# Optimization experiments

Hardware: AMD Instinct MI355X
Metric: run time of the kernel (lower is better)

## Reference

```python
import jax, jax.numpy as jnp
import numpy as np


def _conv(x, w, b=None, stride=1, pad=1):
    y = jax.lax.conv_general_dilated(x, w, (stride, stride), [(pad, pad), (pad, pad)],
                                     dimension_numbers=('NCHW', 'OIHW', 'NCHW'))
    return y if b is None else y + b[None, :, None, None]


def _relu(x):
    return jnp.maximum(x, 0.0)


def _slice(grid, guide):
    # grid: [N,C=12,D=8,Hg=16,Wg=16]; guide: [N,H,W] in [0,1]
    # Emulates F.grid_sample(5D, align_corners=False, padding_mode='border') with
    # coords (x=ww over Wg, y=hh over Hg, z=guide over D).
    N, C, D, Hg, Wg = grid.shape
    H, W = guide.shape[1], guide.shape[2]

    def unnorm(c, size):
        return jnp.clip(((c + 1.0) * size - 1.0) * 0.5, 0.0, size - 1.0)

    ix = unnorm(jnp.linspace(-1.0, 1.0, W), Wg)   # [W]
    iy = unnorm(jnp.linspace(-1.0, 1.0, H), Hg)   # [H]
    iz = unnorm(guide * 2.0 - 1.0, D)             # [N,H,W]
    x0f = jnp.floor(ix); y0f = jnp.floor(iy); z0f = jnp.floor(iz)
    wx = (ix - x0f)[None, :]   # [1,W]
    wy = (iy - y0f)[:, None]   # [H,1]
    wz = iz - z0f              # [N,H,W]
    x0 = jnp.clip(x0f.astype(jnp.int32), 0, Wg - 1); x1 = jnp.clip(x0 + 1, 0, Wg - 1)
    y0 = jnp.clip(y0f.astype(jnp.int32), 0, Hg - 1); y1 = jnp.clip(y0 + 1, 0, Hg - 1)
    z0 = jnp.clip(z0f.astype(jnp.int32), 0, D - 1);  z1 = jnp.clip(z0 + 1, 0, D - 1)

    def sample_one(g, z0n, z1n, wzn):
        # g: [C,D,Hg,Wg]; z0n,z1n,wzn: [H,W]
        def gat(zi, yi, xi):
            return g[:, zi, yi[:, None], xi[None, :]]  # [C,H,W]
        out = jnp.zeros((C, H, W), g.dtype)
        for zi, wzz in ((z0n, 1.0 - wzn), (z1n, wzn)):
            for yi, wyy in ((y0, 1.0 - wy), (y1, wy)):
                for xi, wxx in ((x0, 1.0 - wx), (x1, wx)):
                    out = out + (wzz * wyy * wxx)[None] * gat(zi, yi, xi)
        return out

    return jax.vmap(sample_one, in_axes=(0, 0, 0, 0))(grid, z0, z1, wz)  # [N,12,H,W]


def _forward(lowres, fullres, sw1, sb1, sw2, sb2, sw3, sb3, sw4, sb4,
             gw1, gb1, gw2, gb2, fw3, fb3, fw4, fb4, fw5, fb5,
             lw1, lb1, lw2, pw, pb, M, Mb, thr, slopes, gbias):
    N = lowres.shape[0]
    # Coefficients (low-res CNN)
    x = _relu(_conv(lowres, sw1, sb1, 2))
    x = _relu(_conv(x, sw2, sb2, 2))
    x = _relu(_conv(x, sw3, sb3, 2))
    x = _relu(_conv(x, sw4, sb4, 2))
    splat = x                                  # [N,64,16,16]
    x = _relu(_conv(x, gw1, gb1, 2))
    x = _relu(_conv(x, gw2, gb2, 2))           # [N,64,4,4]
    x = x.reshape(N, -1)
    x = _relu(x @ fw3.T + fb3)
    x = _relu(x @ fw4.T + fb4)
    glob = x @ fw5.T + fb5                     # [N,64]
    loc = _conv(_relu(_conv(splat, lw1, lb1)), lw2, None)
    fusion = _relu(loc + glob[:, :, None, None])
    grid = _conv(fusion, pw, pb, 1, 0).reshape(N, 12, 8, 16, 16)

    # Guide (full-res pointwise network)
    f = fullres.transpose(0, 2, 3, 1)          # [N,H,W,3]
    g = f @ M + Mb                             # [N,H,W,3]
    g = jnp.sum(slopes * _relu(g[..., None] - thr), axis=4)  # [N,H,W,3]
    guide = jnp.clip(jnp.mean(g, axis=3) + gbias, 0.0, 1.0)  # [N,H,W]

    sliced = _slice(grid, guide)               # [N,12,H,W]
    rr = jnp.sum(fullres * sliced[:, 0:3], axis=1) + sliced[:, 3]
    gg = jnp.sum(fullres * sliced[:, 4:7], axis=1) + sliced[:, 7]
    bb = jnp.sum(fullres * sliced[:, 8:11], axis=1) + sliced[:, 11]
    return jnp.stack([rr, gg, bb], axis=1)


def setup_inputs():
    key = jax.random.key(0)
    ks = jax.random.split(key, 32)
    r = lambda i, shape, s=0.1: jax.random.normal(ks[i], shape, jnp.float32) * s
    return {
        'lowres': jax.random.uniform(ks[0], (2, 3, 256, 256), dtype=jnp.float32),
        'fullres': jax.random.uniform(ks[1], (2, 3, 1024, 1024), dtype=jnp.float32),
        'sw1': r(2, (8, 3, 3, 3)),   'sb1': r(3, (8,), 0.01),
        'sw2': r(4, (16, 8, 3, 3)),  'sb2': r(5, (16,), 0.01),
        'sw3': r(6, (32, 16, 3, 3)), 'sb3': r(7, (32,), 0.01),
        'sw4': r(8, (64, 32, 3, 3)), 'sb4': r(9, (64,), 0.01),
        'gw1': r(10, (64, 64, 3, 3)), 'gb1': r(11, (64,), 0.01),
        'gw2': r(12, (64, 64, 3, 3)), 'gb2': r(13, (64,), 0.01),
        'fw3': r(14, (256, 1024), 0.05), 'fb3': r(15, (256,), 0.01),
        'fw4': r(16, (128, 256), 0.05),  'fb4': r(17, (128,), 0.01),
        'fw5': r(18, (64, 128), 0.05),   'fb5': r(19, (64,), 0.01),
        'lw1': r(20, (64, 64, 3, 3)), 'lb1': r(21, (64,), 0.01),
        'lw2': r(22, (64, 64, 3, 3)),
        'pw': r(23, (96, 64, 1, 1)), 'pb': r(24, (96,), 0.01),
        'M': jnp.eye(3, dtype=jnp.float32) + r(25, (3, 3), 0.0001),
        'Mb': jnp.zeros((3,), jnp.float32),
        'thr': jax.random.uniform(ks[26], (1, 1, 3, 16), dtype=jnp.float32),
        'slopes': r(27, (1, 1, 1, 3, 16), 0.3),
        'gbias': jnp.asarray(0.05, jnp.float32),
    }


def reference(lowres, fullres, sw1, sb1, sw2, sb2, sw3, sb3, sw4, sb4,
              gw1, gb1, gw2, gb2, fw3, fb3, fw4, fb4, fw5, fb5,
              lw1, lb1, lw2, pw, pb, M, Mb, thr, slopes, gbias):
    return _forward(lowres, fullres, sw1, sb1, sw2, sb2, sw3, sb3, sw4, sb4,
                    gw1, gb1, gw2, gb2, fw3, fb3, fw4, fb4, fw5, fb5,
                    lw1, lb1, lw2, pw, pb, M, Mb, thr, slopes, gbias)
```

## Files before the change

kernel.cpp:

```cpp
#include <hip/hip_runtime.h>


#define LUT_NB   512
#define LUT_LO   (-0.25f)
#define LUT_BIN  (1.5f / LUT_NB)
#define LUT_INV  (LUT_NB / 1.5f)

__global__ void __launch_bounds__(256) conv12_k(
    const float* __restrict__ lowres,
    const float* __restrict__ sw1, const float* __restrict__ sb1,
    const float* __restrict__ sw2, const float* __restrict__ sb2,
    const float* __restrict__ thr, const float* __restrict__ slp,
    const float* __restrict__ fw3, const float* __restrict__ fw4,
    const float* __restrict__ fw5,
    float* __restrict__ x2, float2* __restrict__ lut,
    float* __restrict__ fwt3, float* __restrict__ fwt4,
    float* __restrict__ fwt5)
{
    __shared__ float s_x1[9 * 9 * 8];
    const int tid  = threadIdx.x;
    const int n    = blockIdx.x >> 8;
    const int tile = blockIdx.x & 255;
    const int ty   = tile >> 4, tx = tile & 15;

    {
        int tg = blockIdx.x * 256 + tid;
        #pragma unroll
        for (int r = 0; r < 2; ++r) {
            int e = tg + r * 131072;
            int o = e & 255, k = e >> 8;
            fwt3[e] = fw3[o * 1024 + k];
        }
        if (tg < 32768) {
            int o = tg & 127, k = tg >> 7;
            fwt4[tg] = fw4[o * 256 + k];
        }
        if (tg < 8192) {
            int o = tg & 63, k = tg >> 6;
            fwt5[tg] = fw5[o * 128 + k];
        }
    }

    if (blockIdx.x == 0) {
        for (int e = tid; e < 3 * LUT_NB; e += 256) {
            int j = e >> 9;
            int i = e & (LUT_NB - 1);
            float xl = LUT_LO + i * LUT_BIN;
            float xh = xl + LUT_BIN;
            float a = 0.0f, c = 0.0f;
            #pragma unroll
            for (int k = 0; k < 16; ++k) {
                float tt = thr[j * 16 + k], ss = slp[j * 16 + k];
                a = fmaf(ss, fmaxf(xl - tt, 0.0f), a);
                c = fmaf(ss, fmaxf(xh - tt, 0.0f), c);
            }
            lut[e] = make_float2(a, c - a);
        }
    }

    const int b1h = 8 * ty - 1, b1w = 8 * tx - 1;

    for (int i = tid; i < 648; i += 256) {
        int c   = i & 7;
        int pos = i >> 3;
        int lw  = pos % 9, lh = pos / 9;
        int gh  = b1h + lh, gw = b1w + lw;
        float v = 0.0f;
        if (gh >= 0 && gh < 128 && gw >= 0 && gw < 128) {
            float acc = sb1[c];
            #pragma unroll
            for (int ci = 0; ci < 3; ++ci) {
                const float* ib = lowres + ((size_t)(n * 3 + ci)) * 65536;
                const float* wb = sw1 + ((size_t)c * 3 + ci) * 9;
                #pragma unroll
                for (int kh = 0; kh < 3; ++kh) {
                    int ih = 2 * gh - 1 + kh;
                    if (ih < 0 || ih >= 256) continue;
                    #pragma unroll
                    for (int kw = 0; kw < 3; ++kw) {
                        int iw = 2 * gw - 1 + kw;
                        if (iw < 0 || iw >= 256) continue;
                        acc = fmaf(ib[ih * 256 + iw], wb[kh * 3 + kw], acc);
                    }
                }
            }
            v = fmaxf(acc, 0.0f);
        }
        s_x1[i] = v;
    }
    __syncthreads();

    {
        int co  = tid & 15;
        int pos = tid >> 4;
        int ooh = pos >> 2, oow = pos & 3;
        int oh  = 4 * ty + ooh, ow = 4 * tx + oow;
        float acc = sb2[co];
        const float* wb = sw2 + (size_t)co * 72;
        #pragma unroll
        for (int kh = 0; kh < 3; ++kh) {
            #pragma unroll
            for (int kw = 0; kw < 3; ++kw) {
                const float* xp = &s_x1[((2 * ooh + kh) * 9 + (2 * oow + kw)) * 8];
                const float* wp = wb + kh * 3 + kw;
                #pragma unroll
                for (int ci = 0; ci < 8; ++ci)
                    acc = fmaf(xp[ci], wp[ci * 9], acc);
            }
        }
        x2[((size_t)(n * 64 + oh) * 64 + ow) * 16 + co] = fmaxf(acc, 0.0f);
    }
}

template <int CIN>
__global__ void convw_hwc_k(const float* __restrict__ in, const float* __restrict__ w,
                            const float* __restrict__ b, float* __restrict__ out,
                            int N, int Hin, int Win, int Cout, int Hout, int Wout,
                            int stride, int do_relu)
{
    constexpr int OPW = 64 / CIN;
    int lane = threadIdx.x & 63;
    int wid  = (blockIdx.x * blockDim.x + threadIdx.x) >> 6;
    int sub  = lane / CIN;
    int cl   = lane % CIN;
    int o    = wid * OPW + sub;
    int total = N * Hout * Wout * Cout;

    float acc = 0.0f;
    if (o < total) {
        int co  = o % Cout;
        int pix = o / Cout;
        int ow  = pix % Wout;
        int oh  = (pix / Wout) % Hout;
        int n   = pix / (Wout * Hout);
        const float* wb = w + ((size_t)co * CIN + cl) * 9;
        #pragma unroll
        for (int kh = 0; kh < 3; ++kh) {
            int ih = oh * stride - 1 + kh;
            if (ih < 0 || ih >= Hin) continue;
            const float* ib = in + (((size_t)(n * Hin + ih)) * Win) * CIN + cl;
            #pragma unroll
            for (int kw = 0; kw < 3; ++kw) {
                int iw = ow * stride - 1 + kw;
                if (iw < 0 || iw >= Win) continue;
                acc = fmaf(ib[(size_t)iw * CIN], wb[kh * 3 + kw], acc);
            }
        }
    }
    #pragma unroll
    for (int off = CIN / 2; off >= 1; off >>= 1)
        acc += __shfl_xor(acc, off, 64);

    if (o < total && cl == 0) {
        if (b) acc += b[o % Cout];
        if (do_relu) acc = fmaxf(acc, 0.0f);
        out[o] = acc;
    }
}

__device__ __forceinline__ void convw64_one(const float* __restrict__ in,
                                            const float* __restrict__ wgt,
                                            const float* __restrict__ bias,
                                            float* __restrict__ out,
                                            int o, int Hin, int Win, int Wout,
                                            int stride, bool relu, int lane)
{
    int co  = o & 63;
    int pix = o >> 6;
    int ow  = pix % Wout;
    int oh  = pix / Wout;
    const float* wb = wgt + ((size_t)co * 64 + lane) * 9;
    float acc = 0.0f;
    #pragma unroll
    for (int kh = 0; kh < 3; ++kh) {
        int ih = oh * stride - 1 + kh;
        if (ih < 0 || ih >= Hin) continue;
        const float* ib = in + ((size_t)ih * Win) * 64 + lane;
        #pragma unroll
        for (int kw = 0; kw < 3; ++kw) {
            int iw = ow * stride - 1 + kw;
            if (iw < 0 || iw >= Win) continue;
            acc = fmaf(ib[(size_t)iw * 64], wb[kh * 3 + kw], acc);
        }
    }
    #pragma unroll
    for (int off = 32; off >= 1; off >>= 1)
        acc += __shfl_xor(acc, off, 64);
    if (lane == 0) {
        if (bias) acc += bias[co];
        if (relu) acc = fmaxf(acc, 0.0f);
        out[o] = acc;
    }
}

__global__ void l1_g1_k(const float* __restrict__ splat,
                        const float* __restrict__ lw1, const float* __restrict__ lb1,
                        const float* __restrict__ gw1, const float* __restrict__ gb1,
                        float* __restrict__ l1, float* __restrict__ g1)
{
    int lane = threadIdx.x & 63;
    int W = (blockIdx.x * blockDim.x + threadIdx.x) >> 6;
    if (W < 32768) {
        int n = W >> 14, o = W & 16383;
        convw64_one(splat + (size_t)n * 16384, lw1, lb1, l1 + (size_t)n * 16384,
                    o, 16, 16, 16, 1, true, lane);
    } else {
        int W2 = W - 32768;
        if (W2 >= 8192) return;
        int n = W2 >> 12, o = W2 & 4095;
        convw64_one(splat + (size_t)n * 16384, gw1, gb1, g1 + (size_t)n * 4096,
                    o, 16, 16, 8, 2, true, lane);
    }
}

__global__ void loc_g2_k(const float* __restrict__ l1, const float* __restrict__ lw2,
                         const float* __restrict__ g1, const float* __restrict__ gw2,
                         const float* __restrict__ gb2,
                         float* __restrict__ loc, float* __restrict__ g2)
{
    int lane = threadIdx.x & 63;
    int W = (blockIdx.x * blockDim.x + threadIdx.x) >> 6;
    if (W < 32768) {
        int n = W >> 14, o = W & 16383;
        convw64_one(l1 + (size_t)n * 16384, lw2, nullptr, loc + (size_t)n * 16384,
                    o, 16, 16, 16, 1, false, lane);
    } else {
        int W2 = W - 32768;
        if (W2 >= 2048) return;
        int n = W2 >> 10, o = W2 & 1023;
        convw64_one(g1 + (size_t)n * 4096, gw2, gb2, g2 + (size_t)n * 1024,
                    o, 8, 8, 4, 2, true, lane);
    }
}

__global__ void __launch_bounds__(1024) fcfusion96_k(
    const float* __restrict__ g2,
    const float* __restrict__ fwt3, const float* __restrict__ fb3,
    const float* __restrict__ fwt4, const float* __restrict__ fb4,
    const float* __restrict__ fwt5, const float* __restrict__ fb5,
    const float* __restrict__ loc,
    const float* __restrict__ pw, const float* __restrict__ pb,
    float* __restrict__ gridc)
{
    __shared__ float s_in[1024];
    __shared__ float s_p[1024];
    __shared__ float s_f3[256];
    __shared__ float s_f4[128];
    __shared__ float s_gl[64];

    const int tid = threadIdx.x;
    const int n   = blockIdx.x / 48;
    const int q   = blockIdx.x % 48;

    if (tid < 1024)
        s_in[tid] = g2[(size_t)n * 1024 + (tid & 15) * 64 + (tid >> 4)];
    __syncthreads();

    {
        int o = tid & 255, part = tid >> 8;
        const float* wp = fwt3 + (size_t)(part * 256) * 256 + o;
        const float* ip = s_in + part * 256;
        float acc = 0.0f;
        #pragma unroll 8
        for (int k = 0; k < 256; ++k)
            acc = fmaf(wp[k * 256], ip[k], acc);
        s_p[tid] = acc;
    }
    __syncthreads();
    if (tid < 256)
        s_f3[tid] = fmaxf(fb3[tid] + s_p[tid] + s_p[256 + tid] +
                          s_p[512 + tid] + s_p[768 + tid], 0.0f);
    __syncthreads();

    if (tid < 512) {
        int o = tid & 127, part = tid >> 7;
        const float* wp = fwt4 + (size_t)(part * 64) * 128 + o;
        const float* ip = s_f3 + part * 64;
        float acc = 0.0f;
        #pragma unroll 8
        for (int k = 0; k < 64; ++k)
            acc = fmaf(wp[k * 128], ip[k], acc);
        s_p[tid] = acc;
    }
    __syncthreads();
    if (tid < 128)
        s_f4[tid] = fmaxf(fb4[tid] + s_p[tid] + s_p[128 + tid] +
                          s_p[256 + tid] + s_p[384 + tid], 0.0f);
    __syncthreads();

    if (tid < 256) {
        int o = tid & 63, part = tid >> 6;
        const float* wp = fwt5 + (size_t)(part * 32) * 64 + o;
        const float* ip = s_f4 + part * 32;
        float acc = 0.0f;
        #pragma unroll 8
        for (int k = 0; k < 32; ++k)
            acc = fmaf(wp[k * 64], ip[k], acc);
        s_p[tid] = acc;
    }
    __syncthreads();
    if (tid < 64)
        s_gl[tid] = fb5[tid] + s_p[tid] + s_p[64 + tid] +
                    s_p[128 + tid] + s_p[192 + tid];
    __syncthreads();

    if (tid < 512) {
        int idx = q * 512 + tid;
        int c   = idx % 12;
        int zp  = idx / 12;
        int p   = zp & 255;
        int z   = zp >> 8;
        int co  = c * 8 + z;
        const float4* lp = (const float4*)(loc + ((size_t)n * 256 + p) * 64);
        const float4* gp = (const float4*)s_gl;
        const float4* wp = (const float4*)(pw + (size_t)co * 64);
        float acc = pb[co];
        #pragma unroll
        for (int i = 0; i < 16; ++i) {
            float4 l = lp[i], g = gp[i], w = wp[i];
            acc = fmaf(fmaxf(l.x + g.x, 0.0f), w.x, acc);
            acc = fmaf(fmaxf(l.y + g.y, 0.0f), w.y, acc);
            acc = fmaf(fmaxf(l.z + g.z, 0.0f), w.z, acc);
            acc = fmaf(fmaxf(l.w + g.w, 0.0f), w.w, acc);
        }
        gridc[(size_t)n * 24576 + idx] = acc;
    }
}

__global__ void __launch_bounds__(256) guide_slice_lut_k(
    const float* __restrict__ fullres,
    const float* __restrict__ gridc,
    const float2* __restrict__ lutg,
    const float* __restrict__ M, const float* __restrict__ Mb,
    const float* __restrict__ gbias,
    float* __restrict__ out)
{
    const int W = 1024, H = 1024;
    __shared__ float  ly[1536];
    __shared__ float2 lutS[3 * LUT_NB];

    int h = blockIdx.x & 1023;
    int n = blockIdx.x >> 10;

    float iy = fminf(fmaxf((float)h * (16.0f / (H - 1)) - 0.5f, 0.0f), 15.0f);
    float y0f = floorf(iy);
    float wy  = iy - y0f;
    int y0 = (int)y0f, y1 = min(y0 + 1, 15);

    const float* gn = gridc + (size_t)n * 24576;
    for (int i = threadIdx.x; i < 1536; i += 256) {
        int z   = i / 192;
        int rem = i - z * 192;
        float a = gn[z * 3072 + y0 * 192 + rem];
        float b = gn[z * 3072 + y1 * 192 + rem];
        ly[i] = fmaf(wy, b - a, a);
        lutS[i] = lutg[i];
    }
    __syncthreads();

    float M00 = M[0], M10 = M[3], M20 = M[6];
    float M01 = M[1], M11 = M[4], M21 = M[7];
    float M02 = M[2], M12 = M[5], M22 = M[8];
    float Mb0 = Mb[0], Mb1 = Mb[1], Mb2 = Mb[2];
    float gb  = gbias[0];

    int w0 = (int)threadIdx.x * 4;
    size_t plane = (size_t)H * W;
    size_t base  = (size_t)n * 3 * plane + (size_t)h * W + w0;
    float4 R  = *(const float4*)&fullres[base];
    float4 G  = *(const float4*)&fullres[base + plane];
    float4 Bc = *(const float4*)&fullres[base + 2 * plane];

    const float4* L = (const float4*)ly;

    float4 RR, GG, BB;
    float* rr = &RR.x; float* gg = &GG.x; float* bb = &BB.x;
    const float* rp = &R.x; const float* gp2 = &G.x; const float* bp = &Bc.x;

    #pragma unroll
    for (int p = 0; p < 4; ++p) {
        float r = rp[p], g = gp2[p], bc = bp[p];
        int w = w0 + p;

        float g0 = fmaf(r, M00, fmaf(g, M10, fmaf(bc, M20, Mb0)));
        float g1 = fmaf(r, M01, fmaf(g, M11, fmaf(bc, M21, Mb1)));
        float g2 = fmaf(r, M02, fmaf(g, M12, fmaf(bc, M22, Mb2)));
        float sum = 0.0f;
        {
            float t0 = fminf(fmaxf((g0 - LUT_LO) * LUT_INV, 0.0f), LUT_NB - 1.0f);
            int i0 = (int)t0; float f0 = t0 - (float)i0;
            float2 e0 = lutS[i0];
            sum += fmaf(f0, e0.y, e0.x);
            float t1 = fminf(fmaxf((g1 - LUT_LO) * LUT_INV, 0.0f), LUT_NB - 1.0f);
            int i1 = (int)t1; float f1 = t1 - (float)i1;
            float2 e1 = lutS[LUT_NB + i1];
            sum += fmaf(f1, e1.y, e1.x);
            float t2 = fminf(fmaxf((g2 - LUT_LO) * LUT_INV, 0.0f), LUT_NB - 1.0f);
            int i2 = (int)t2; float f2 = t2 - (float)i2;
            float2 e2 = lutS[2 * LUT_NB + i2];
            sum += fmaf(f2, e2.y, e2.x);
        }
        float guide = fminf(fmaxf(sum * (1.0f / 3.0f) + gb, 0.0f), 1.0f);

        float ix = fminf(fmaxf((float)w * (16.0f / (W - 1)) - 0.5f, 0.0f), 15.0f);
        float iz = fminf(fmaxf(8.0f * guide - 0.5f, 0.0f), 7.0f);
        float x0f = floorf(ix), z0f = floorf(iz);
        float wx = ix - x0f, wz = iz - z0f;
        int x0 = (int)x0f; int x1 = min(x0 + 1, 15);
        int z0 = (int)z0f; int z1 = min(z0 + 1, 7);
        float mx = 1.f - wx, mz = 1.f - wz;

        int n00 = (z0 * 16 + x0) * 3, n01 = (z0 * 16 + x1) * 3;
        int n10 = (z1 * 16 + x0) * 3, n11 = (z1 * 16 + x1) * 3;
        float W00 = mz * mx, W01 = mz * wx, W10 = wz * mx, W11 = wz * wx;

        float4 A0 = {0.f, 0.f, 0.f, 0.f}, A1 = A0, A2 = A0;
        auto nodeacc = [&](int nb, float wt) {
            float4 v0 = L[nb], v1 = L[nb + 1], v2 = L[nb + 2];
            A0.x = fmaf(wt, v0.x, A0.x); A0.y = fmaf(wt, v0.y, A0.y);
            A0.z = fmaf(wt, v0.z, A0.z); A0.w = fmaf(wt, v0.w, A0.w);
            A1.x = fmaf(wt, v1.x, A1.x); A1.y = fmaf(wt, v1.y, A1.y);
            A1.z = fmaf(wt, v1.z, A1.z); A1.w = fmaf(wt, v1.w, A1.w);
            A2.x = fmaf(wt, v2.x, A2.x); A2.y = fmaf(wt, v2.y, A2.y);
            A2.z = fmaf(wt, v2.z, A2.z); A2.w = fmaf(wt, v2.w, A2.w);
        };
        nodeacc(n00, W00);
        nodeacc(n01, W01);
        nodeacc(n10, W10);
        nodeacc(n11, W11);

        rr[p] = fmaf(r, A0.x, fmaf(g, A0.y, fmaf(bc, A0.z, A0.w)));
        gg[p] = fmaf(r, A1.x, fmaf(g, A1.y, fmaf(bc, A1.z, A1.w)));
        bb[p] = fmaf(r, A2.x, fmaf(g, A2.y, fmaf(bc, A2.z, A2.w)));
    }

    *(float4*)&out[base]             = RR;
    *(float4*)&out[base + plane]     = GG;
    *(float4*)&out[base + 2 * plane] = BB;
}

extern "C" void kernel_launch(void* const* d_in, const int* in_sizes, int n_in,
                              void* d_out, int out_size, void* d_ws, size_t ws_size,
                              hipStream_t stream)
{
    const float* lowres  = (const float*)d_in[0];
    const float* fullres = (const float*)d_in[1];
    const float* sw1 = (const float*)d_in[2];  const float* sb1 = (const float*)d_in[3];
    const float* sw2 = (const float*)d_in[4];  const float* sb2 = (const float*)d_in[5];
    const float* sw3 = (const float*)d_in[6];  const float* sb3 = (const float*)d_in[7];
    const float* sw4 = (const float*)d_in[8];  const float* sb4 = (const float*)d_in[9];
    const float* gw1 = (const float*)d_in[10]; const float* gb1 = (const float*)d_in[11];
    const float* gw2 = (const float*)d_in[12]; const float* gb2 = (const float*)d_in[13];
    const float* fw3 = (const float*)d_in[14]; const float* fb3 = (const float*)d_in[15];
    const float* fw4 = (const float*)d_in[16]; const float* fb4 = (const float*)d_in[17];
    const float* fw5 = (const float*)d_in[18]; const float* fb5 = (const float*)d_in[19];
    const float* lw1 = (const float*)d_in[20]; const float* lb1 = (const float*)d_in[21];
    const float* lw2 = (const float*)d_in[22];
    const float* pw  = (const float*)d_in[23]; const float* pb  = (const float*)d_in[24];
    const float* M   = (const float*)d_in[25]; const float* Mb  = (const float*)d_in[26];
    const float* thr = (const float*)d_in[27]; const float* slp = (const float*)d_in[28];
    const float* gbias = (const float*)d_in[29];

    const int N = 2, B = 256;
    auto wblk = [](int total_out, int opw) {
        int waves = (total_out + opw - 1) / opw;
        return (waves * 64 + 255) / 256;
    };

    float* ws    = (float*)d_ws;
    float* x2    = ws;
    float* x3    = x2 + 131072;
    float* splat = x3 + 65536;
    float* g1    = splat + 32768;
    float* g2    = g1 + 8192;
    float* l1    = g2 + 2048;
    float* loc   = l1 + 32768;
    float* gridc = loc + 32768;
    float2* lutg = (float2*)(gridc + 49152);
    float* fwt3  = (float*)(lutg + 1536);
    float* fwt4  = fwt3 + 262144;
    float* fwt5  = fwt4 + 32768;

    conv12_k<<<512, 256, 0, stream>>>(lowres, sw1, sb1, sw2, sb2, thr, slp,
        fw3, fw4, fw5, x2, lutg, fwt3, fwt4, fwt5);
    convw_hwc_k<16><<<wblk(2*32*32*32, 4), B, 0, stream>>>(x2, sw3, sb3, x3,
        N, 64, 64, 32, 32, 32, 2, 1);
    convw_hwc_k<32><<<wblk(2*16*16*64, 2), B, 0, stream>>>(x3, sw4, sb4, splat,
        N, 32, 32, 64, 16, 16, 2, 1);
    l1_g1_k<<<10240, 256, 0, stream>>>(splat, lw1, lb1, gw1, gb1, l1, g1);
    loc_g2_k<<<8704, 256, 0, stream>>>(l1, lw2, g1, gw2, gb2, loc, g2);
    fcfusion96_k<<<96, 1024, 0, stream>>>(g2, fwt3, fb3, fwt4, fb4, fwt5, fb5,
        loc, pw, pb, gridc);
    guide_slice_lut_k<<<2048, 256, 0, stream>>>(fullres, gridc, lutg, M, Mb,
        gbias, (float*)d_out);
}
```

Before: 121.5 us.

## Fuse conv3 into conv12, merge global path with FC, fold pointwise into slice

Conv3 now runs inside the first low-res kernel using a larger halo tile held in shared memory, which removes the x2 round trip and one launch. The global conv2 and the FC chain move into two extra blocks of the loc conv kernel, each doing a single-block FC without split-K. The pointwise fusion projection moves into the slice kernel, where each block recomputes the grid rows it needs. This cuts two launches and the gridc buffer, at the cost of recomputing the 1x1 projection in every slice block and serialising the FC work onto one block per image.

```diff
diff --git a/kernel.cpp b/kernel.cpp
--- a/kernel.cpp
+++ b/kernel.cpp
@@ -6,18 +6,20 @@
 #define LUT_BIN  (1.5f / LUT_NB)
 #define LUT_INV  (LUT_NB / 1.5f)
 
-__global__ void __launch_bounds__(256) conv12_k(
+__global__ void __launch_bounds__(256) conv123_k(
     const float* __restrict__ lowres,
     const float* __restrict__ sw1, const float* __restrict__ sb1,
     const float* __restrict__ sw2, const float* __restrict__ sb2,
+    const float* __restrict__ sw3, const float* __restrict__ sb3,
     const float* __restrict__ thr, const float* __restrict__ slp,
     const float* __restrict__ fw3, const float* __restrict__ fw4,
     const float* __restrict__ fw5,
-    float* __restrict__ x2, float2* __restrict__ lut,
+    float* __restrict__ x3, float2* __restrict__ lut,
     float* __restrict__ fwt3, float* __restrict__ fwt4,
     float* __restrict__ fwt5)
 {
-    __shared__ float s_x1[9 * 9 * 8];
+    __shared__ float s_x1[11 * 11 * 8];
+    __shared__ float s_x2[5 * 5 * 16];
     const int tid  = threadIdx.x;
     const int n    = blockIdx.x >> 8;
     const int tile = blockIdx.x & 255;
@@ -40,7 +42,6 @@
             fwt5[tg] = fw5[o * 128 + k];
         }
     }
-
     if (blockIdx.x == 0) {
         for (int e = tid; e < 3 * LUT_NB; e += 256) {
             int j = e >> 9;
@@ -58,12 +59,13 @@
         }
     }
 
-    const int b1h = 8 * ty - 1, b1w = 8 * tx - 1;
-
-    for (int i = tid; i < 648; i += 256) {
+    const int b1h = 8 * ty - 3, b1w = 8 * tx - 3;
+    const int b2h = 4 * ty - 1, b2w = 4 * tx - 1;
+
+    for (int i = tid; i < 968; i += 256) {
         int c   = i & 7;
         int pos = i >> 3;
-        int lw  = pos % 9, lh = pos / 9;
+        int lw  = pos % 11, lh = pos / 11;
         int gh  = b1h + lh, gw = b1w + lw;
         float v = 0.0f;
         if (gh >= 0 && gh < 128 && gw >= 0 && gw < 128) {
@@ -90,25 +92,51 @@
     }
     __syncthreads();
 
-    {
-        int co  = tid & 15;
-        int pos = tid >> 4;
-        int ooh = pos >> 2, oow = pos & 3;
-        int oh  = 4 * ty + ooh, ow = 4 * tx + oow;
-        float acc = sb2[co];
-        const float* wb = sw2 + (size_t)co * 72;
+    for (int i = tid; i < 400; i += 256) {
+        int c   = i & 15;
+        int pos = i >> 4;
+        int lw  = pos % 5, lh = pos / 5;
+        int gh  = b2h + lh, gw = b2w + lw;
+        float v = 0.0f;
+        if (gh >= 0 && gh < 64 && gw >= 0 && gw < 64) {
+            float acc = sb2[c];
+            const float* wb = sw2 + (size_t)c * 72;
+            #pragma unroll
+            for (int kh = 0; kh < 3; ++kh) {
+                #pragma unroll
+                for (int kw = 0; kw < 3; ++kw) {
+                    const float* xp = &s_x1[((2 * lh + kh) * 11 + 2 * lw + kw) * 8];
+                    const float* wp = wb + kh * 3 + kw;
+                    #pragma unroll
+                    for (int ci = 0; ci < 8; ++ci)
+                        acc = fmaf(xp[ci], wp[ci * 9], acc);
+                }
+            }
+            v = fmaxf(acc, 0.0f);
+        }
+        s_x2[i] = v;
+    }
+    __syncthreads();
+
+    if (tid < 128) {
+        int c   = tid & 31;
+        int pos = tid >> 5;
+        int lh  = pos >> 1, lw = pos & 1;
+        int gh  = 2 * ty + lh, gw = 2 * tx + lw;
+        float acc = sb3[c];
+        const float* wb = sw3 + (size_t)c * 144;
         #pragma unroll
         for (int kh = 0; kh < 3; ++kh) {
             #pragma unroll
             for (int kw = 0; kw < 3; ++kw) {
-                const float* xp = &s_x1[((2 * ooh + kh) * 9 + (2 * oow + kw)) * 8];
+                const float* xp = &s_x2[((2 * lh + kh) * 5 + 2 * lw + kw) * 16];
                 const float* wp = wb + kh * 3 + kw;
                 #pragma unroll
-                for (int ci = 0; ci < 8; ++ci)
+                for (int ci = 0; ci < 16; ++ci)
                     acc = fmaf(xp[ci], wp[ci * 9], acc);
             }
         }
-        x2[((size_t)(n * 64 + oh) * 64 + ow) * 16 + co] = fmaxf(acc, 0.0f);
+        x3[((size_t)(n * 32 + gh) * 32 + gw) * 32 + c] = fmaxf(acc, 0.0f);
     }
 }
 
@@ -213,123 +241,92 @@
     }
 }
 
-__global__ void loc_g2_k(const float* __restrict__ l1, const float* __restrict__ lw2,
-                         const float* __restrict__ g1, const float* __restrict__ gw2,
-                         const float* __restrict__ gb2,
-                         float* __restrict__ loc, float* __restrict__ g2)
-{
-    int lane = threadIdx.x & 63;
-    int W = (blockIdx.x * blockDim.x + threadIdx.x) >> 6;
-    if (W < 32768) {
+__global__ void __launch_bounds__(256) loc_gfc_k(
+    const float* __restrict__ l1, const float* __restrict__ lw2,
+    const float* __restrict__ g1,
+    const float* __restrict__ gw2, const float* __restrict__ gb2,
+    const float* __restrict__ fwt3, const float* __restrict__ fb3,
+    const float* __restrict__ fwt4, const float* __restrict__ fb4,
+    const float* __restrict__ fwt5, const float* __restrict__ fb5,
+    float* __restrict__ loc, float* __restrict__ glob)
+{
+    __shared__ float s_g1[4096];
+    __shared__ float s_g2[1024];
+    __shared__ float s_f3[256];
+    __shared__ float s_f4[128];
+
+    const int tid  = threadIdx.x;
+    const int lane = tid & 63;
+
+    if (blockIdx.x < 8192) {
+        int W = blockIdx.x * 4 + (tid >> 6);
         int n = W >> 14, o = W & 16383;
         convw64_one(l1 + (size_t)n * 16384, lw2, nullptr, loc + (size_t)n * 16384,
                     o, 16, 16, 16, 1, false, lane);
-    } else {
-        int W2 = W - 32768;
-        if (W2 >= 2048) return;
-        int n = W2 >> 10, o = W2 & 1023;
-        convw64_one(g1 + (size_t)n * 4096, gw2, gb2, g2 + (size_t)n * 1024,
-                    o, 8, 8, 4, 2, true, lane);
-    }
-}
-
-__global__ void __launch_bounds__(1024) fcfusion96_k(
-    const float* __restrict__ g2,
-    const float* __restrict__ fwt3, const float* __restrict__ fb3,
-    const float* __restrict__ fwt4, const float* __restrict__ fb4,
-    const float* __restrict__ fwt5, const float* __restrict__ fb5,
-    const float* __restrict__ loc,
-    const float* __restrict__ pw, const float* __restrict__ pb,
-    float* __restrict__ gridc)
-{
-    __shared__ float s_in[1024];
-    __shared__ float s_p[1024];
-    __shared__ float s_f3[256];
-    __shared__ float s_f4[128];
-    __shared__ float s_gl[64];
-
-    const int tid = threadIdx.x;
-    const int n   = blockIdx.x / 48;
-    const int q   = blockIdx.x % 48;
-
-    if (tid < 1024)
-        s_in[tid] = g2[(size_t)n * 1024 + (tid & 15) * 64 + (tid >> 4)];
+        return;
+    }
+
+    const int n = blockIdx.x - 8192;
+    for (int i = tid; i < 4096; i += 256)
+        s_g1[i] = g1[(size_t)n * 4096 + i];
+    __syncthreads();
+
+    for (int o = tid; o < 1024; o += 256) {
+        int co  = o & 63;
+        int pos = o >> 6;
+        int oh  = pos >> 2, ow = pos & 3;
+        float acc = gb2[co];
+        const float* wb = gw2 + (size_t)co * 576;
+        #pragma unroll
+        for (int kh = 0; kh < 3; ++kh) {
+            int ih = 2 * oh - 1 + kh;
+            if (ih < 0 || ih >= 8) continue;
+            #pragma unroll
+            for (int kw = 0; kw < 3; ++kw) {
+                int iw = 2 * ow - 1 + kw;
+                if (iw < 0 || iw >= 8) continue;
+                const float* gp = &s_g1[(ih * 8 + iw) * 64];
+                const float* wp = wb + kh * 3 + kw;
+                #pragma unroll
+                for (int ci = 0; ci < 64; ++ci)
+                    acc = fmaf(gp[ci], wp[ci * 9], acc);
+            }
+        }
+        s_g2[pos * 64 + co] = fmaxf(acc, 0.0f);
+    }
     __syncthreads();
 
     {
-        int o = tid & 255, part = tid >> 8;
-        const float* wp = fwt3 + (size_t)(part * 256) * 256 + o;
-        const float* ip = s_in + part * 256;
-        float acc = 0.0f;
+        float acc = fb3[tid];
+        #pragma unroll 8
+        for (int j = 0; j < 1024; ++j)
+            acc = fmaf(s_g2[(j & 15) * 64 + (j >> 4)], fwt3[j * 256 + tid], acc);
+        s_f3[tid] = fmaxf(acc, 0.0f);
+    }
+    __syncthreads();
+
+    if (tid < 128) {
+        float acc = fb4[tid];
         #pragma unroll 8
         for (int k = 0; k < 256; ++k)
-            acc = fmaf(wp[k * 256], ip[k], acc);
-        s_p[tid] = acc;
-    }
-    __syncthreads();
-    if (tid < 256)
-        s_f3[tid] = fmaxf(fb3[tid] + s_p[tid] + s_p[256 + tid] +
-                          s_p[512 + tid] + s_p[768 + tid], 0.0f);
-    __syncthreads();
-
-    if (tid < 512) {
-        int o = tid & 127, part = tid >> 7;
-        const float* wp = fwt4 + (size_t)(part * 64) * 128 + o;
-        const float* ip = s_f3 + part * 64;
-        float acc = 0.0f;
+            acc = fmaf(s_f3[k], fwt4[k * 128 + tid], acc);
+        s_f4[tid] = fmaxf(acc, 0.0f);
+    }
+    __syncthreads();
+
+    if (tid < 64) {
+        float acc = fb5[tid];
         #pragma unroll 8
-        for (int k = 0; k < 64; ++k)
-            acc = fmaf(wp[k * 128], ip[k], acc);
-        s_p[tid] = acc;
-    }
-    __syncthreads();
-    if (tid < 128)
-        s_f4[tid] = fmaxf(fb4[tid] + s_p[tid] + s_p[128 + tid] +
-                          s_p[256 + tid] + s_p[384 + tid], 0.0f);
-    __syncthreads();
-
-    if (tid < 256) {
-        int o = tid & 63, part = tid >> 6;
-        const float* wp = fwt5 + (size_t)(part * 32) * 64 + o;
-        const float* ip = s_f4 + part * 32;
-        float acc = 0.0f;
-        #pragma unroll 8
-        for (int k = 0; k < 32; ++k)
-            acc = fmaf(wp[k * 64], ip[k], acc);
-        s_p[tid] = acc;
-    }
-    __syncthreads();
-    if (tid < 64)
-        s_gl[tid] = fb5[tid] + s_p[tid] + s_p[64 + tid] +
-                    s_p[128 + tid] + s_p[192 + tid];
-    __syncthreads();
-
-    if (tid < 512) {
-        int idx = q * 512 + tid;
-        int c   = idx % 12;
-        int zp  = idx / 12;
-        int p   = zp & 255;
-        int z   = zp >> 8;
-        int co  = c * 8 + z;
-        const float4* lp = (const float4*)(loc + ((size_t)n * 256 + p) * 64);
-        const float4* gp = (const float4*)s_gl;
-        const float4* wp = (const float4*)(pw + (size_t)co * 64);
-        float acc = pb[co];
-        #pragma unroll
-        for (int i = 0; i < 16; ++i) {
-            float4 l = lp[i], g = gp[i], w = wp[i];
-            acc = fmaf(fmaxf(l.x + g.x, 0.0f), w.x, acc);
-            acc = fmaf(fmaxf(l.y + g.y, 0.0f), w.y, acc);
-            acc = fmaf(fmaxf(l.z + g.z, 0.0f), w.z, acc);
-            acc = fmaf(fmaxf(l.w + g.w, 0.0f), w.w, acc);
-        }
-        gridc[(size_t)n * 24576 + idx] = acc;
-    }
-}
-
-__global__ void __launch_bounds__(256) guide_slice_lut_k(
+        for (int k = 0; k < 128; ++k)
+            acc = fmaf(s_f4[k], fwt5[k * 64 + tid], acc);
+        glob[(size_t)n * 64 + tid] = acc;
+    }
+}
+
+__global__ void __launch_bounds__(256) slice_k(
     const float* __restrict__ fullres,
-    const float* __restrict__ gridc,
+    const float* __restrict__ loc, const float* __restrict__ glob,
+    const float* __restrict__ pw, const float* __restrict__ pb,
     const float2* __restrict__ lutg,
     const float* __restrict__ M, const float* __restrict__ Mb,
     const float* __restrict__ gbias,
@@ -337,6 +334,7 @@
 {
     const int W = 1024, H = 1024;
     __shared__ float  ly[1536];
+    __shared__ float  gtmp[2 * 16 * 96];
     __shared__ float2 lutS[3 * LUT_NB];
 
     int h = blockIdx.x & 1023;
@@ -347,14 +345,50 @@
     float wy  = iy - y0f;
     int y0 = (int)y0f, y1 = min(y0 + 1, 15);
 
-    const float* gn = gridc + (size_t)n * 24576;
+    for (int i = threadIdx.x; i < 3 * LUT_NB; i += 256)
+        lutS[i] = lutg[i];
+
+    {
+        int t   = threadIdx.x;
+        int pos = t >> 3;
+        int grp = t & 7;
+        int yi  = pos >> 4;
+        int x   = pos & 15;
+        int y   = yi ? y1 : y0;
+
+        float fus[64];
+        const float4* lp = (const float4*)(loc + ((size_t)(n * 16 + y) * 16 + x) * 64);
+        const float4* gp = (const float4*)(glob + (size_t)n * 64);
+        #pragma unroll
+        for (int i = 0; i < 16; ++i) {
+            float4 l = lp[i], g = gp[i];
+            fus[4 * i + 0] = fmaxf(l.x + g.x, 0.0f);
+            fus[4 * i + 1] = fmaxf(l.y + g.y, 0.0f);
+            fus[4 * i + 2] = fmaxf(l.z + g.z, 0.0f);
+            fus[4 * i + 3] = fmaxf(l.w + g.w, 0.0f);
+        }
+        #pragma unroll
+        for (int k = 0; k < 12; ++k) {
+            int co = grp * 12 + k;
+            const float* wp = pw + (size_t)co * 64;
+            float acc = pb[co];
+            #pragma unroll
+            for (int i = 0; i < 64; ++i)
+                acc = fmaf(fus[i], wp[i], acc);
+            gtmp[(yi * 16 + x) * 96 + co] = acc;
+        }
+    }
+    __syncthreads();
+
     for (int i = threadIdx.x; i < 1536; i += 256) {
         int z   = i / 192;
         int rem = i - z * 192;
-        float a = gn[z * 3072 + y0 * 192 + rem];
-        float b = gn[z * 3072 + y1 * 192 + rem];
+        int x   = rem / 12;
+        int c   = rem - x * 12;
+        int co  = c * 8 + z;
+        float a = gtmp[x * 96 + co];
+        float b = gtmp[(16 + x) * 96 + co];
         ly[i] = fmaf(wy, b - a, a);
-        lutS[i] = lutg[i];
     }
     __syncthreads();
 
@@ -468,29 +502,24 @@
     };
 
     float* ws    = (float*)d_ws;
-    float* x2    = ws;
-    float* x3    = x2 + 131072;
+    float* x3    = ws;
     float* splat = x3 + 65536;
     float* g1    = splat + 32768;
-    float* g2    = g1 + 8192;
-    float* l1    = g2 + 2048;
+    float* l1    = g1 + 8192;
     float* loc   = l1 + 32768;
-    float* gridc = loc + 32768;
-    float2* lutg = (float2*)(gridc + 49152);
+    float* glob  = loc + 32768;
+    float2* lutg = (float2*)(glob + 128);
     float* fwt3  = (float*)(lutg + 1536);
     float* fwt4  = fwt3 + 262144;
     float* fwt5  = fwt4 + 32768;
 
-    conv12_k<<<512, 256, 0, stream>>>(lowres, sw1, sb1, sw2, sb2, thr, slp,
-        fw3, fw4, fw5, x2, lutg, fwt3, fwt4, fwt5);
-    convw_hwc_k<16><<<wblk(2*32*32*32, 4), B, 0, stream>>>(x2, sw3, sb3, x3,
-        N, 64, 64, 32, 32, 32, 2, 1);
+    conv123_k<<<512, 256, 0, stream>>>(lowres, sw1, sb1, sw2, sb2, sw3, sb3,
+        thr, slp, fw3, fw4, fw5, x3, lutg, fwt3, fwt4, fwt5);
     convw_hwc_k<32><<<wblk(2*16*16*64, 2), B, 0, stream>>>(x3, sw4, sb4, splat,
         N, 32, 32, 64, 16, 16, 2, 1);
     l1_g1_k<<<10240, 256, 0, stream>>>(splat, lw1, lb1, gw1, gb1, l1, g1);
-    loc_g2_k<<<8704, 256, 0, stream>>>(l1, lw2, g1, gw2, gb2, loc, g2);
-    fcfusion96_k<<<96, 1024, 0, stream>>>(g2, fwt3, fb3, fwt4, fb4, fwt5, fb5,
-        loc, pw, pb, gridc);
-    guide_slice_lut_k<<<2048, 256, 0, stream>>>(fullres, gridc, lutg, M, Mb,
-        gbias, (float*)d_out);
-}
+    loc_gfc_k<<<8194, 256, 0, stream>>>(l1, lw2, g1, gw2, gb2,
+        fwt3, fb3, fwt4, fb4, fwt5, fb5, loc, glob);
+    slice_k<<<2048, 256, 0, stream>>>(fullres, loc, glob, pw, pb, lutg,
+        M, Mb, gbias, (float*)d_out);
+}
```

Result: slower. 466.3 us (+283.7%).

## Fuse third strided conv into conv1-2 kernel with halo recomputation

Applied to the files above, without the earlier changes.

Extends the fused low-res conv kernel to also compute conv3, keeping conv1 and conv2 outputs in shared memory with enlarged halos (11x11 and 5x5 tiles). This removes one kernel launch and the global write/read of the 64x64x16 intermediate. In exchange each block recomputes overlapping halo regions of conv1/conv2, and only 128 of 256 threads do the conv3 stage.

```diff
diff --git a/kernel.cpp b/kernel.cpp
--- a/kernel.cpp
+++ b/kernel.cpp
@@ -6,18 +6,20 @@
 #define LUT_BIN  (1.5f / LUT_NB)
 #define LUT_INV  (LUT_NB / 1.5f)
 
-__global__ void __launch_bounds__(256) conv12_k(
+__global__ void __launch_bounds__(256) conv123_k(
     const float* __restrict__ lowres,
     const float* __restrict__ sw1, const float* __restrict__ sb1,
     const float* __restrict__ sw2, const float* __restrict__ sb2,
+    const float* __restrict__ sw3, const float* __restrict__ sb3,
     const float* __restrict__ thr, const float* __restrict__ slp,
     const float* __restrict__ fw3, const float* __restrict__ fw4,
     const float* __restrict__ fw5,
-    float* __restrict__ x2, float2* __restrict__ lut,
+    float* __restrict__ x3, float2* __restrict__ lut,
     float* __restrict__ fwt3, float* __restrict__ fwt4,
     float* __restrict__ fwt5)
 {
-    __shared__ float s_x1[9 * 9 * 8];
+    __shared__ float s_x1[11 * 11 * 8];
+    __shared__ float s_x2[5 * 5 * 16];
     const int tid  = threadIdx.x;
     const int n    = blockIdx.x >> 8;
     const int tile = blockIdx.x & 255;
@@ -40,7 +42,6 @@
             fwt5[tg] = fw5[o * 128 + k];
         }
     }
-
     if (blockIdx.x == 0) {
         for (int e = tid; e < 3 * LUT_NB; e += 256) {
             int j = e >> 9;
@@ -58,12 +59,13 @@
         }
     }
 
-    const int b1h = 8 * ty - 1, b1w = 8 * tx - 1;
-
-    for (int i = tid; i < 648; i += 256) {
+    const int b1h = 8 * ty - 3, b1w = 8 * tx - 3;
+    const int b2h = 4 * ty - 1, b2w = 4 * tx - 1;
+
+    for (int i = tid; i < 968; i += 256) {
         int c   = i & 7;
         int pos = i >> 3;
-        int lw  = pos % 9, lh = pos / 9;
+        int lw  = pos % 11, lh = pos / 11;
         int gh  = b1h + lh, gw = b1w + lw;
         float v = 0.0f;
         if (gh >= 0 && gh < 128 && gw >= 0 && gw < 128) {
@@ -90,25 +92,51 @@
     }
     __syncthreads();
 
-    {
-        int co  = tid & 15;
-        int pos = tid >> 4;
-        int ooh = pos >> 2, oow = pos & 3;
-        int oh  = 4 * ty + ooh, ow = 4 * tx + oow;
-        float acc = sb2[co];
-        const float* wb = sw2 + (size_t)co * 72;
+    for (int i = tid; i < 400; i += 256) {
+        int c   = i & 15;
+        int pos = i >> 4;
+        int lw  = pos % 5, lh = pos / 5;
+        int gh  = b2h + lh, gw = b2w + lw;
+        float v = 0.0f;
+        if (gh >= 0 && gh < 64 && gw >= 0 && gw < 64) {
+            float acc = sb2[c];
+            const float* wb = sw2 + (size_t)c * 72;
+            #pragma unroll
+            for (int kh = 0; kh < 3; ++kh) {
+                #pragma unroll
+                for (int kw = 0; kw < 3; ++kw) {
+                    const float* xp = &s_x1[((2 * lh + kh) * 11 + 2 * lw + kw) * 8];
+                    const float* wp = wb + kh * 3 + kw;
+                    #pragma unroll
+                    for (int ci = 0; ci < 8; ++ci)
+                        acc = fmaf(xp[ci], wp[ci * 9], acc);
+                }
+            }
+            v = fmaxf(acc, 0.0f);
+        }
+        s_x2[i] = v;
+    }
+    __syncthreads();
+
+    if (tid < 128) {
+        int c   = tid & 31;
+        int pos = tid >> 5;
+        int lh  = pos >> 1, lw = pos & 1;
+        int gh  = 2 * ty + lh, gw = 2 * tx + lw;
+        float acc = sb3[c];
+        const float* wb = sw3 + (size_t)c * 144;
         #pragma unroll
         for (int kh = 0; kh < 3; ++kh) {
             #pragma unroll
             for (int kw = 0; kw < 3; ++kw) {
-                const float* xp = &s_x1[((2 * ooh + kh) * 9 + (2 * oow + kw)) * 8];
+                const float* xp = &s_x2[((2 * lh + kh) * 5 + 2 * lw + kw) * 16];
                 const float* wp = wb + kh * 3 + kw;
                 #pragma unroll
-                for (int ci = 0; ci < 8; ++ci)
+                for (int ci = 0; ci < 16; ++ci)
                     acc = fmaf(xp[ci], wp[ci * 9], acc);
             }
         }
-        x2[((size_t)(n * 64 + oh) * 64 + ow) * 16 + co] = fmaxf(acc, 0.0f);
+        x3[((size_t)(n * 32 + gh) * 32 + gw) * 32 + c] = fmaxf(acc, 0.0f);
     }
 }
 
@@ -468,8 +496,7 @@
     };
 
     float* ws    = (float*)d_ws;
-    float* x2    = ws;
-    float* x3    = x2 + 131072;
+    float* x3    = ws;
     float* splat = x3 + 65536;
     float* g1    = splat + 32768;
     float* g2    = g1 + 8192;
@@ -481,10 +508,8 @@
     float* fwt4  = fwt3 + 262144;
     float* fwt5  = fwt4 + 32768;
 
-    conv12_k<<<512, 256, 0, stream>>>(lowres, sw1, sb1, sw2, sb2, thr, slp,
-        fw3, fw4, fw5, x2, lutg, fwt3, fwt4, fwt5);
-    convw_hwc_k<16><<<wblk(2*32*32*32, 4), B, 0, stream>>>(x2, sw3, sb3, x3,
-        N, 64, 64, 32, 32, 32, 2, 1);
+    conv123_k<<<512, 256, 0, stream>>>(lowres, sw1, sb1, sw2, sb2, sw3, sb3,
+        thr, slp, fw3, fw4, fw5, x3, lutg, fwt3, fwt4, fwt5);
     convw_hwc_k<32><<<wblk(2*16*16*64, 2), B, 0, stream>>>(x3, sw4, sb4, splat,
         N, 32, 32, 64, 16, 16, 2, 1);
     l1_g1_k<<<10240, 256, 0, stream>>>(splat, lw1, lb1, gw1, gb1, l1, g1);
```

After: 117.3 us. 1.04x faster.
